# Optimization experiments

Hardware: AMD Instinct MI355X
Metric: run time of the kernel (lower is better)

The kernel has to match this reference:

```python
import jax, jax.numpy as jnp
import numpy as np

B, N1, N2 = 16, 256, 256
FA, FE = 128, 128  # n_atom_feature, n_edge_feature


def setup_inputs() -> dict:
    key = jax.random.key(0)
    ks = jax.random.split(key, 8)
    x1 = jax.random.normal(ks[0], (B, N1, FA), dtype=jnp.float32)
    x2 = jax.random.normal(ks[1], (B, N2, FA), dtype=jnp.float32)
    edge = jax.random.normal(ks[2], (B, N1, N2, FE), dtype=jnp.float32)
    valid_edge = jax.random.randint(ks[3], (B, N1, N2), 0, 2).astype(jnp.float32)
    s_w = 1.0 / np.sqrt(FA)
    s_m = 1.0 / np.sqrt(FE + FA)
    W_w = jax.random.uniform(ks[4], (FA, FA), jnp.float32, -s_w, s_w)      # [in, out]
    W_b = jax.random.uniform(ks[5], (FA,), jnp.float32, -s_w, s_w)
    M_w = jax.random.uniform(ks[6], (FE + FA, FA), jnp.float32, -s_m, s_m)  # [in, out]
    M_b = jax.random.uniform(ks[7], (FA,), jnp.float32, -s_m, s_m)
    return {"x1": x1, "x2": x2, "edge": edge, "valid_edge": valid_edge,
            "W_w": W_w, "W_b": W_b, "M_w": M_w, "M_b": M_b}


def reference(x1, x2, edge, valid_edge, W_w, W_b, M_w, M_b):
    # m1 = W(x1): [B, N1, FA]
    m1 = jnp.einsum('bif,fg->big', x1, W_w) + W_b
    # M(new_edge) without materializing concat: split M into x2-part and edge-part.
    # new_edge = cat([broadcast(x2) -> [B,N1,N2,FA], edge], -1)
    Mw_x2 = M_w[:FA]    # [FA, FA]
    Mw_e = M_w[FA:]     # [FE, FA]
    me = jnp.einsum('bije,eg->bijg', edge, Mw_e)                 # [B,N1,N2,FA]
    mx2 = jnp.einsum('bjf,fg->bjg', x2, Mw_x2)                   # [B,N2,FA]
    m_edge = me + mx2[:, None, :, :] + M_b                       # [B,N1,N2,FA]
    # mask-multiply then max over neighbor axis (axis=2), as in the original
    m2 = jnp.max(m_edge * valid_edge[..., None], axis=2)         # [B,N1,FA]
    return jax.nn.relu(m1 + m2)
```

## Files before the change

kernel.cpp:

```cpp
#include <hip/hip_runtime.h>
#include <hip/hip_bf16.h>

#define BB 16
#define N1 256
#define N2 256
#define FA 128
#define FE 128

typedef __attribute__((ext_vector_type(8))) short bf16x8;
typedef __attribute__((ext_vector_type(4))) float f32x4;

static __device__ __forceinline__ unsigned short f2bf(float f) {
    union { float f; unsigned int u; } v; v.f = f;
    unsigned int u = v.u;
    unsigned int r = (u + 0x7FFFu + ((u >> 16) & 1u)) >> 16;
    return (unsigned short)r;
}

static __device__ __forceinline__ bf16x8 pack8(float4 lo, float4 hi) {
    bf16x8 r;
    r[0] = (short)f2bf(lo.x); r[1] = (short)f2bf(lo.y);
    r[2] = (short)f2bf(lo.z); r[3] = (short)f2bf(lo.w);
    r[4] = (short)f2bf(hi.x); r[5] = (short)f2bf(hi.y);
    r[6] = (short)f2bf(hi.z); r[7] = (short)f2bf(hi.w);
    return r;
}

__global__ __launch_bounds__(128) void prep_gemm(const float* __restrict__ x,
                                                 const float* __restrict__ W,
                                                 const float* __restrict__ bias,
                                                 float* __restrict__ out) {
    __shared__ float xs[8][128];
    const int r0 = blockIdx.x * 8;
    const int g = threadIdx.x;
    #pragma unroll
    for (int r = 0; r < 8; ++r)
        xs[r][g] = x[(size_t)(r0 + r) * FA + g];
    __syncthreads();
    float acc[8];
    const float bv = bias[g];
    #pragma unroll
    for (int r = 0; r < 8; ++r) acc[r] = bv;
    #pragma unroll 8
    for (int f = 0; f < 128; ++f) {
        const float wv = W[f * FA + g];
        #pragma unroll
        for (int r = 0; r < 8; ++r) acc[r] += xs[r][f] * wv;
    }
    #pragma unroll
    for (int r = 0; r < 8; ++r)
        out[(size_t)(r0 + r) * FA + g] = acc[r];
}

__global__ __launch_bounds__(128) void prep_gemm_T(const float* __restrict__ x,
                                                   const float* __restrict__ W,
                                                   const float* __restrict__ bias,
                                                   float* __restrict__ outT) {
    __shared__ float xs[8][128];
    const int r0 = blockIdx.x * 8;
    const int b = r0 >> 8;
    const int j0 = r0 & 255;
    const int g = threadIdx.x;
    #pragma unroll
    for (int r = 0; r < 8; ++r)
        xs[r][g] = x[(size_t)(r0 + r) * FA + g];
    __syncthreads();
    float acc[8];
    const float bv = bias[g];
    #pragma unroll
    for (int r = 0; r < 8; ++r) acc[r] = bv;
    #pragma unroll 8
    for (int f = 0; f < 128; ++f) {
        const float wv = W[f * FA + g];
        #pragma unroll
        for (int r = 0; r < 8; ++r) acc[r] += xs[r][f] * wv;
    }
    float4 v0 = {acc[0], acc[1], acc[2], acc[3]};
    float4 v1 = {acc[4], acc[5], acc[6], acc[7]};
    float4* dst = (float4*)&outT[(size_t)(b * 128 + g) * 256 + j0];
    dst[0] = v0;
    dst[1] = v1;
}

__global__ __launch_bounds__(256) void prep_wt(const float* __restrict__ Mw,
                                               unsigned short* __restrict__ wT) {
    const int idx = blockIdx.x * 256 + threadIdx.x;
    const int g = idx >> 7, e = idx & 127;
    wT[idx] = f2bf(Mw[(size_t)(FA + e) * FA + g]);
}

__global__ __launch_bounds__(256, 3) void edge_main(
    const float* __restrict__ edge,
    const float* __restrict__ valid,
    const float* __restrict__ mx2bT,
    const unsigned short* __restrict__ wT,
    float* __restrict__ out)
{
    __shared__ __align__(16) unsigned short ebuf[2][2048];

    const int tid = threadIdx.x;
    const int wv = tid >> 6;
    const int lane = tid & 63;
    const int n = lane & 15, q = lane >> 4;
    const int bi = blockIdx.x;
    const int b = bi >> 8;

    bf16x8 bF[2][4];
    #pragma unroll
    for (int tt = 0; tt < 2; ++tt) {
        const int t = wv * 2 + tt;
        #pragma unroll
        for (int s = 0; s < 4; ++s)
            bF[tt][s] = *(const bf16x8*)&wT[(t * 16 + n) * FE + s * 32 + q * 8];
    }

    const float* eb  = edge + (size_t)bi * (N2 * FE);
    const float* mxT = mx2bT + (size_t)b * (N2 * FA);
    const float* vb  = valid + (size_t)bi * N2;

    const int sj = tid >> 4;
    const int se = (tid & 15) * 8;
    const float* sg = eb + (size_t)sj * FE + se;
    char* ebase = (char*)&ebuf[0][0];
    const int sphys = (tid * 16) ^ ((sj & 7) << 4);

    {
        float4 v0 = *(const float4*)(sg);
        float4 v1 = *(const float4*)(sg + 4);
        *(bf16x8*)(ebase + sphys) = pack8(v0, v1);
    }
    __syncthreads();

    float runmax[2] = {-3.0e38f, -3.0e38f};

    const int lq = n * 256 + q * 16;
    const int xsw = (n & 7) << 4;

    for (int strip = 0; strip < 16; ++strip) {
        const int j0 = strip * 16;
        const bool more = (strip + 1) < 16;

        float4 p0, p1;
        if (more) {
            const float* nsg = sg + (size_t)(j0 + 16) * FE;
            p0 = *(const float4*)(nsg);
            p1 = *(const float4*)(nsg + 4);
        }

        const float4 vld = *(const float4*)(vb + j0 + q * 4);
        float4 mxv[2];
        #pragma unroll
        for (int tt = 0; tt < 2; ++tt) {
            const int t = wv * 2 + tt;
            mxv[tt] = *(const float4*)(mxT + (size_t)(t * 16 + n) * N2 + j0 + q * 4);
        }

        char* cbuf = ebase + (strip & 1) * 4096;
        bf16x8 aF[4];
        #pragma unroll
        for (int s = 0; s < 4; ++s)
            aF[s] = *(const bf16x8*)(cbuf + ((lq + s * 64) ^ xsw));

        #pragma unroll
        for (int tt = 0; tt < 2; ++tt) {
            f32x4 acc = {0.f, 0.f, 0.f, 0.f};
            #pragma unroll
            for (int s = 0; s < 4; ++s)
                acc = __builtin_amdgcn_mfma_f32_16x16x32_bf16(aF[s], bF[tt][s], acc, 0, 0, 0);
            float v0 = (acc[0] + mxv[tt].x) * vld.x;
            float v1 = (acc[1] + mxv[tt].y) * vld.y;
            float v2 = (acc[2] + mxv[tt].z) * vld.z;
            float v3 = (acc[3] + mxv[tt].w) * vld.w;
            runmax[tt] = fmaxf(runmax[tt], fmaxf(fmaxf(v0, v1), fmaxf(v2, v3)));
        }

        if (more) {
            *(bf16x8*)(ebase + (((strip + 1) & 1) * 4096) + sphys) = pack8(p0, p1);
        }
        __syncthreads();
    }

    #pragma unroll
    for (int tt = 0; tt < 2; ++tt) {
        float m = runmax[tt];
        m = fmaxf(m, __shfl_xor(m, 16, 64));
        m = fmaxf(m, __shfl_xor(m, 32, 64));
        if (lane < 16) {
            const int t = wv * 2 + tt;
            const size_t o = (size_t)bi * FA + t * 16 + lane;
            out[o] = fmaxf(out[o] + m, 0.0f);
        }
    }
}

extern "C" void kernel_launch(void* const* d_in, const int* in_sizes, int n_in,
                              void* d_out, int out_size, void* d_ws, size_t ws_size,
                              hipStream_t stream) {
    const float* x1    = (const float*)d_in[0];
    const float* x2    = (const float*)d_in[1];
    const float* edge  = (const float*)d_in[2];
    const float* valid = (const float*)d_in[3];
    const float* W_w   = (const float*)d_in[4];
    const float* W_b   = (const float*)d_in[5];
    const float* M_w   = (const float*)d_in[6];
    const float* M_b   = (const float*)d_in[7];
    float* out = (float*)d_out;

    unsigned short* wT = (unsigned short*)d_ws;
    float* mx2bT = (float*)((char*)d_ws + 32768);

    prep_gemm<<<BB * N1 / 8, 128, 0, stream>>>(x1, W_w, W_b, out);
    prep_gemm_T<<<BB * N2 / 8, 128, 0, stream>>>(x2, M_w, M_b, mx2bT);
    prep_wt<<<64, 256, 0, stream>>>(M_w, wT);
    edge_main<<<BB * N1, 256, 0, stream>>>(edge, valid, mx2bT, wT, out);
}
```

Before: 753.7 us.

## Merge prep kernels and process 32-row edge strips per barrier

Fuses the three preprocessing kernels into one launch that dispatches on block index, removing two launch gaps. The main edge kernel now stages 32 neighbor rows per iteration instead of 16. This halves the number of strips and block barriers and puts more loads in flight per thread. It also interleaves the two MFMA chains and raises the occupancy hint to 4 blocks per CU, at the cost of doubled LDS and more registers per thread.

```diff
diff --git a/kernel.cpp b/kernel.cpp
--- a/kernel.cpp
+++ b/kernel.cpp
@@ -26,13 +26,29 @@
     return r;
 }
 
-__global__ __launch_bounds__(128) void prep_gemm(const float* __restrict__ x,
-                                                 const float* __restrict__ W,
-                                                 const float* __restrict__ bias,
-                                                 float* __restrict__ out) {
+__global__ __launch_bounds__(128) void prep_all(
+    const float* __restrict__ x1, const float* __restrict__ x2,
+    const float* __restrict__ W_w, const float* __restrict__ W_b,
+    const float* __restrict__ M_w, const float* __restrict__ M_b,
+    float* __restrict__ out, float* __restrict__ mx2bT,
+    unsigned short* __restrict__ wT) {
+    const int blk = blockIdx.x;
+    const int g = threadIdx.x;
+
+    if (blk >= 1024) {
+        const int idx = (blk - 1024) * 128 + g;
+        const int gg = idx >> 7, e = idx & 127;
+        wT[idx] = f2bf(M_w[(size_t)(FA + e) * FA + gg]);
+        return;
+    }
+
     __shared__ float xs[8][128];
-    const int r0 = blockIdx.x * 8;
-    const int g = threadIdx.x;
+    const bool isT = (blk >= 512);
+    const int r0 = (isT ? blk - 512 : blk) * 8;
+    const float* x = isT ? x2 : x1;
+    const float* W = isT ? M_w : W_w;
+    const float* bias = isT ? M_b : W_b;
+
     #pragma unroll
     for (int r = 0; r < 8; ++r)
         xs[r][g] = x[(size_t)(r0 + r) * FA + g];
@@ -47,56 +63,28 @@
         #pragma unroll
         for (int r = 0; r < 8; ++r) acc[r] += xs[r][f] * wv;
     }
-    #pragma unroll
-    for (int r = 0; r < 8; ++r)
-        out[(size_t)(r0 + r) * FA + g] = acc[r];
-}
-
-__global__ __launch_bounds__(128) void prep_gemm_T(const float* __restrict__ x,
-                                                   const float* __restrict__ W,
-                                                   const float* __restrict__ bias,
-                                                   float* __restrict__ outT) {
-    __shared__ float xs[8][128];
-    const int r0 = blockIdx.x * 8;
-    const int b = r0 >> 8;
-    const int j0 = r0 & 255;
-    const int g = threadIdx.x;
-    #pragma unroll
-    for (int r = 0; r < 8; ++r)
-        xs[r][g] = x[(size_t)(r0 + r) * FA + g];
-    __syncthreads();
-    float acc[8];
-    const float bv = bias[g];
-    #pragma unroll
-    for (int r = 0; r < 8; ++r) acc[r] = bv;
-    #pragma unroll 8
-    for (int f = 0; f < 128; ++f) {
-        const float wv = W[f * FA + g];
+    if (!isT) {
         #pragma unroll
-        for (int r = 0; r < 8; ++r) acc[r] += xs[r][f] * wv;
-    }
-    float4 v0 = {acc[0], acc[1], acc[2], acc[3]};
-    float4 v1 = {acc[4], acc[5], acc[6], acc[7]};
-    float4* dst = (float4*)&outT[(size_t)(b * 128 + g) * 256 + j0];
-    dst[0] = v0;
-    dst[1] = v1;
-}
-
-__global__ __launch_bounds__(256) void prep_wt(const float* __restrict__ Mw,
-                                               unsigned short* __restrict__ wT) {
-    const int idx = blockIdx.x * 256 + threadIdx.x;
-    const int g = idx >> 7, e = idx & 127;
-    wT[idx] = f2bf(Mw[(size_t)(FA + e) * FA + g]);
-}
-
-__global__ __launch_bounds__(256, 3) void edge_main(
+        for (int r = 0; r < 8; ++r)
+            out[(size_t)(r0 + r) * FA + g] = acc[r];
+    } else {
+        const int b = r0 >> 8, j0 = r0 & 255;
+        float4 v0 = {acc[0], acc[1], acc[2], acc[3]};
+        float4 v1 = {acc[4], acc[5], acc[6], acc[7]};
+        float4* dst = (float4*)&mx2bT[(size_t)(b * 128 + g) * 256 + j0];
+        dst[0] = v0;
+        dst[1] = v1;
+    }
+}
+
+__global__ __launch_bounds__(256, 4) void edge_main(
     const float* __restrict__ edge,
     const float* __restrict__ valid,
     const float* __restrict__ mx2bT,
     const unsigned short* __restrict__ wT,
     float* __restrict__ out)
 {
-    __shared__ __align__(16) unsigned short ebuf[2][2048];
+    __shared__ __align__(16) unsigned short ebuf[2][4096];
 
     const int tid = threadIdx.x;
     const int wv = tid >> 6;
@@ -105,13 +93,11 @@
     const int bi = blockIdx.x;
     const int b = bi >> 8;
 
-    bf16x8 bF[2][4];
+    bf16x8 bF0[4], bF1[4];
     #pragma unroll
-    for (int tt = 0; tt < 2; ++tt) {
-        const int t = wv * 2 + tt;
-        #pragma unroll
-        for (int s = 0; s < 4; ++s)
-            bF[tt][s] = *(const bf16x8*)&wT[(t * 16 + n) * FE + s * 32 + q * 8];
+    for (int s = 0; s < 4; ++s) {
+        bF0[s] = *(const bf16x8*)&wT[((wv * 2 + 0) * 16 + n) * FE + s * 32 + q * 8];
+        bF1[s] = *(const bf16x8*)&wT[((wv * 2 + 1) * 16 + n) * FE + s * 32 + q * 8];
     }
 
     const float* eb  = edge + (size_t)bi * (N2 * FE);
@@ -122,72 +108,98 @@
     const int se = (tid & 15) * 8;
     const float* sg = eb + (size_t)sj * FE + se;
     char* ebase = (char*)&ebuf[0][0];
-    const int sphys = (tid * 16) ^ ((sj & 7) << 4);
+    const int sw = (sj & 7) << 4;
+    const int sbyte0 = sj * 256 + (tid & 15) * 16;
+    const int sp0 = sbyte0 ^ sw;
+    const int sp1 = (4096 + sbyte0) ^ sw;
 
     {
-        float4 v0 = *(const float4*)(sg);
-        float4 v1 = *(const float4*)(sg + 4);
-        *(bf16x8*)(ebase + sphys) = pack8(v0, v1);
+        float4 a0 = *(const float4*)(sg);
+        float4 a1 = *(const float4*)(sg + 4);
+        float4 b0 = *(const float4*)(sg + 16 * FE);
+        float4 b1 = *(const float4*)(sg + 16 * FE + 4);
+        *(bf16x8*)(ebase + sp0) = pack8(a0, a1);
+        *(bf16x8*)(ebase + sp1) = pack8(b0, b1);
     }
     __syncthreads();
 
-    float runmax[2] = {-3.0e38f, -3.0e38f};
-
-    const int lq = n * 256 + q * 16;
+    float runmax0 = -3.0e38f, runmax1 = -3.0e38f;
+    const int lqb = n * 256 + q * 16;
     const int xsw = (n & 7) << 4;
 
-    for (int strip = 0; strip < 16; ++strip) {
-        const int j0 = strip * 16;
-        const bool more = (strip + 1) < 16;
-
-        float4 p0, p1;
+    for (int strip = 0; strip < 8; ++strip) {
+        const bool more = (strip + 1) < 8;
+        const int j0 = strip * 32;
+
+        float4 pa0, pa1, pb0, pb1;
         if (more) {
-            const float* nsg = sg + (size_t)(j0 + 16) * FE;
-            p0 = *(const float4*)(nsg);
-            p1 = *(const float4*)(nsg + 4);
-        }
-
-        const float4 vld = *(const float4*)(vb + j0 + q * 4);
-        float4 mxv[2];
+            const float* ns = sg + (size_t)(j0 + 32) * FE;
+            pa0 = *(const float4*)(ns);
+            pa1 = *(const float4*)(ns + 4);
+            pb0 = *(const float4*)(ns + 16 * FE);
+            pb1 = *(const float4*)(ns + 16 * FE + 4);
+        }
+
+        char* cbuf = ebase + (strip & 1) * 8192;
+
         #pragma unroll
-        for (int tt = 0; tt < 2; ++tt) {
-            const int t = wv * 2 + tt;
-            mxv[tt] = *(const float4*)(mxT + (size_t)(t * 16 + n) * N2 + j0 + q * 4);
-        }
-
-        char* cbuf = ebase + (strip & 1) * 4096;
-        bf16x8 aF[4];
-        #pragma unroll
-        for (int s = 0; s < 4; ++s)
-            aF[s] = *(const bf16x8*)(cbuf + ((lq + s * 64) ^ xsw));
-
-        #pragma unroll
-        for (int tt = 0; tt < 2; ++tt) {
-            f32x4 acc = {0.f, 0.f, 0.f, 0.f};
+        for (int h = 0; h < 2; ++h) {
+            const int jh = j0 + h * 16;
+            const float4 vld = *(const float4*)(vb + jh + q * 4);
+            const float4 mxv0 = *(const float4*)(mxT + (size_t)((wv * 2 + 0) * 16 + n) * N2 + jh + q * 4);
+            const float4 mxv1 = *(const float4*)(mxT + (size_t)((wv * 2 + 1) * 16 + n) * N2 + jh + q * 4);
+
+            bf16x8 aF[4];
             #pragma unroll
             for (int s = 0; s < 4; ++s)
-                acc = __builtin_amdgcn_mfma_f32_16x16x32_bf16(aF[s], bF[tt][s], acc, 0, 0, 0);
-            float v0 = (acc[0] + mxv[tt].x) * vld.x;
-            float v1 = (acc[1] + mxv[tt].y) * vld.y;
-            float v2 = (acc[2] + mxv[tt].z) * vld.z;
-            float v3 = (acc[3] + mxv[tt].w) * vld.w;
-            runmax[tt] = fmaxf(runmax[tt], fmaxf(fmaxf(v0, v1), fmaxf(v2, v3)));
+                aF[s] = *(const bf16x8*)(cbuf + ((h * 4096 + lqb + s * 64) ^ xsw));
+
+            f32x4 acc0 = {0.f, 0.f, 0.f, 0.f};
+            f32x4 acc1 = {0.f, 0.f, 0.f, 0.f};
+            #pragma unroll
+            for (int s = 0; s < 4; ++s) {
+                acc0 = __builtin_amdgcn_mfma_f32_16x16x32_bf16(aF[s], bF0[s], acc0, 0, 0, 0);
+                acc1 = __builtin_amdgcn_mfma_f32_16x16x32_bf16(aF[s], bF1[s], acc1, 0, 0, 0);
+            }
+            {
+                float v0 = (acc0[0] + mxv0.x) * vld.x;
+                float v1 = (acc0[1] + mxv0.y) * vld.y;
+                float v2 = (acc0[2] + mxv0.z) * vld.z;
+                float v3 = (acc0[3] + mxv0.w) * vld.w;
+                runmax0 = fmaxf(runmax0, fmaxf(fmaxf(v0, v1), fmaxf(v2, v3)));
+            }
+            {
+                float v0 = (acc1[0] + mxv1.x) * vld.x;
+                float v1 = (acc1[1] + mxv1.y) * vld.y;
+                float v2 = (acc1[2] + mxv1.z) * vld.z;
+                float v3 = (acc1[3] + mxv1.w) * vld.w;
+                runmax1 = fmaxf(runmax1, fmaxf(fmaxf(v0, v1), fmaxf(v2, v3)));
+            }
         }
 
         if (more) {
-            *(bf16x8*)(ebase + (((strip + 1) & 1) * 4096) + sphys) = pack8(p0, p1);
-        }
-        __syncthreads();
-    }
-
-    #pragma unroll
-    for (int tt = 0; tt < 2; ++tt) {
-        float m = runmax[tt];
+            char* obuf = ebase + ((strip + 1) & 1) * 8192;
+            *(bf16x8*)(obuf + sp0) = pack8(pa0, pa1);
+            *(bf16x8*)(obuf + sp1) = pack8(pb0, pb1);
+            __syncthreads();
+        }
+    }
+
+    {
+        float m = runmax0;
         m = fmaxf(m, __shfl_xor(m, 16, 64));
         m = fmaxf(m, __shfl_xor(m, 32, 64));
         if (lane < 16) {
-            const int t = wv * 2 + tt;
-            const size_t o = (size_t)bi * FA + t * 16 + lane;
+            const size_t o = (size_t)bi * FA + (wv * 2 + 0) * 16 + lane;
+            out[o] = fmaxf(out[o] + m, 0.0f);
+        }
+    }
+    {
+        float m = runmax1;
+        m = fmaxf(m, __shfl_xor(m, 16, 64));
+        m = fmaxf(m, __shfl_xor(m, 32, 64));
+        if (lane < 16) {
+            const size_t o = (size_t)bi * FA + (wv * 2 + 1) * 16 + lane;
             out[o] = fmaxf(out[o] + m, 0.0f);
         }
     }
@@ -209,8 +221,6 @@
     unsigned short* wT = (unsigned short*)d_ws;
     float* mx2bT = (float*)((char*)d_ws + 32768);
 
-    prep_gemm<<<BB * N1 / 8, 128, 0, stream>>>(x1, W_w, W_b, out);
-    prep_gemm_T<<<BB * N2 / 8, 128, 0, stream>>>(x2, M_w, M_b, mx2bT);
-    prep_wt<<<64, 256, 0, stream>>>(M_w, wT);
+    prep_all<<<1152, 128, 0, stream>>>(x1, x2, W_w, W_b, M_w, M_b, out, mx2bT, wT);
     edge_main<<<BB * N1, 256, 0, stream>>>(edge, valid, mx2bT, wT, out);
 }
```

Result: faster. 721.1 us (-4.3%).
